# Kernel tuning notes

Measured on AMD Instinct MI355X. Metric: run time of the kernel, lower is better.

The kernel has to match this reference:

```python
import jax, jax.numpy as jnp
import numpy as np


def _local_similar(q, k, kH, kW):
    # q, k: [B, C, H, W] -> scores [B, H, W, kH*kW]
    # Matches similar_forward: zero-padded kH x kW neighborhood dot products.
    B, C, H, W = q.shape
    pH, pW = kH // 2, kW // 2
    kp = jnp.pad(k, ((0, 0), (0, 0), (pH, pH), (pW, pW)))
    scores = [
        jnp.einsum('bchw,bchw->bhw', q, kp[:, :, dh:dh + H, dw:dw + W])
        for dh in range(kH) for dw in range(kW)
    ]
    return jnp.stack(scores, axis=-1)


def _local_weighting(v, w, kH, kW):
    # v: [B, C, H, W], w: [B, H, W, kH*kW] -> out [B, C, H, W]
    # Matches weighting_forward: weighted sum over zero-padded neighborhood.
    B, C, H, W = v.shape
    pH, pW = kH // 2, kW // 2
    vp = jnp.pad(v, ((0, 0), (0, 0), (pH, pH), (pW, pW)))
    out = jnp.zeros_like(v)
    idx = 0
    for dh in range(kH):
        for dw in range(kW):
            out = out + w[..., idx][:, None, :, :] * vp[:, :, dh:dh + H, dw:dw + W]
            idx += 1
    return out


def setup_inputs() -> dict:
    key = jax.random.key(0)
    k1, k2, k3, k4 = jax.random.split(key, 4)
    B, C, H, W = 8, 64, 128, 128
    O = 64  # out_channels
    scale = 1.0 / np.sqrt(C).astype(np.float32)
    x = jax.random.normal(k1, (B, C, H, W), jnp.float32)
    W1 = jax.random.normal(k2, (O, C), jnp.float32) * scale  # conv1 (1x1, no bias)
    W2 = jax.random.normal(k3, (O, C), jnp.float32) * scale  # conv2
    W3 = jax.random.normal(k4, (O, C), jnp.float32) * scale  # conv3
    return {"x": x, "W1": W1, "W2": W2, "W3": W3, "kH": 7, "kW": 7}


def reference(x, W1, W2, W3, kH, kW):
    # 1x1 convs == per-pixel channel matmuls
    q = jnp.einsum('oc,bchw->bohw', W1, x)
    k = jnp.einsum('oc,bchw->bohw', W2, x)
    v = jnp.einsum('oc,bchw->bohw', W3, x)
    scores = _local_similar(q, k, kH, kW)          # [B, H, W, kH*kW]
    w = jax.nn.softmax(scores, axis=-1)
    return _local_weighting(v, w, kH, kW)          # [B, O, H, W]
```

## Files before the change

kernel.cpp:

```cpp
#include <hip/hip_runtime.h>
#include <hip/hip_bf16.h>

#define B_ 8
#define C_ 64
#define H_ 128
#define W_ 128
#define HW_ (H_ * W_)

typedef __attribute__((ext_vector_type(8))) short short8;
typedef __attribute__((ext_vector_type(4))) float float4v;
typedef _Float16 f16x2 __attribute__((ext_vector_type(2)));

static __device__ inline unsigned bfbits(float f) {
    __hip_bfloat16 h = __float2bfloat16(f);
    unsigned short s;
    __builtin_memcpy(&s, &h, 2);
    return (unsigned)s;
}

static __device__ inline float dot2(unsigned a, unsigned b, float c) {
    f16x2 ha, hb;
    __builtin_memcpy(&ha, &a, 4);
    __builtin_memcpy(&hb, &b, 4);
#if __has_builtin(__builtin_amdgcn_fdot2)
    return __builtin_amdgcn_fdot2(ha, hb, c, false);
#else
    return fmaf((float)ha.x, (float)hb.x, fmaf((float)ha.y, (float)hb.y, c));
#endif
}

static __device__ inline float2 up2(unsigned u) {
    f16x2 h;
    __builtin_memcpy(&h, &u, 4);
    return make_float2((float)h.x, (float)h.y);
}

__global__ void repack_w(const float* __restrict__ w1, const float* __restrict__ w2,
                         const float* __restrict__ w3,
                         unsigned short* __restrict__ wBhi, unsigned short* __restrict__ wBlo)
{
    const int i = blockIdx.x * 256 + threadIdx.x;
    if (i >= 12288) return;
    const int j = i & 7, lane = (i >> 3) & 63, ks = (i >> 9) & 1, nt = i >> 10;
    const int o = nt * 16 + (lane & 15);
    const int c = ks * 32 + (lane >> 4) * 8 + j;
    const float* wsel = (o < 64) ? w1 : (o < 128) ? w2 : w3;
    const float w = wsel[(o & 63) * 64 + c];
    const unsigned hb = bfbits(w);
    wBhi[i] = (unsigned short)hb;
    wBlo[i] = (unsigned short)bfbits(w - __uint_as_float(hb << 16));
}

__global__ __launch_bounds__(512, 4) void proj_qkv(
    const float* __restrict__ x,
    const unsigned short* __restrict__ wBhi, const unsigned short* __restrict__ wBlo,
    _Float16* __restrict__ q, _Float16* __restrict__ k, _Float16* __restrict__ v)
{
    const int b = blockIdx.y;
    const int px0 = blockIdx.x * 128;
    const int t = threadIdx.x;
    const int lane = t & 63;
    const int wave = t >> 6;
    const int wave_m = wave & 1, wave_n = wave >> 1;
    const int n = lane & 15, kg = lane >> 4;

    float4v acc[3][4];
    #pragma unroll
    for (int tnt = 0; tnt < 3; ++tnt)
        #pragma unroll
        for (int mt = 0; mt < 4; ++mt)
            acc[tnt][mt] = (float4v){0.f, 0.f, 0.f, 0.f};

    const float* xb = x + (size_t)b * C_ * HW_;
    const int pxl = px0 + wave_m * 64 + n;

    #pragma unroll
    for (int ks = 0; ks < 2; ++ks) {
        short8 ahi[4], alo[4];
        #pragma unroll
        for (int mt = 0; mt < 4; ++mt) {
            #pragma unroll
            for (int j = 0; j < 8; ++j) {
                const int c = ks * 32 + kg * 8 + j;
                const float f = xb[(size_t)c * HW_ + pxl + mt * 16];
                const unsigned hb = bfbits(f);
                ahi[mt][j] = (short)hb;
                alo[mt][j] = (short)bfbits(f - __uint_as_float(hb << 16));
            }
        }
        #pragma unroll
        for (int tnt = 0; tnt < 3; ++tnt) {
            const int gnt = wave_n * 3 + tnt;
            const size_t bidx = (((size_t)gnt * 2 + ks) * 64 + lane) * 8;
            short8 bh, bl;
            {
                const uint4 uh = *(const uint4*)(wBhi + bidx);
                const uint4 ul = *(const uint4*)(wBlo + bidx);
                __builtin_memcpy(&bh, &uh, 16);
                __builtin_memcpy(&bl, &ul, 16);
            }
            #pragma unroll
            for (int mt = 0; mt < 4; ++mt) {
                acc[tnt][mt] = __builtin_amdgcn_mfma_f32_16x16x32_bf16(
                    ahi[mt], bh, acc[tnt][mt], 0, 0, 0);
                acc[tnt][mt] = __builtin_amdgcn_mfma_f32_16x16x32_bf16(
                    alo[mt], bh, acc[tnt][mt], 0, 0, 0);
                acc[tnt][mt] = __builtin_amdgcn_mfma_f32_16x16x32_bf16(
                    ahi[mt], bl, acc[tnt][mt], 0, 0, 0);
            }
        }
    }

    #pragma unroll
    for (int tnt = 0; tnt < 3; ++tnt) {
        const int gnt = wave_n * 3 + tnt;
        _Float16* base = (gnt < 4) ? q : (gnt < 8) ? k : v;
        const int chunk = gnt & 3;
        #pragma unroll
        for (int mt = 0; mt < 4; ++mt) {
            const int pxm = px0 + wave_m * 64 + mt * 16 + kg * 4;
            const float4v d = acc[tnt][mt];
            _Float16* p = base + (((size_t)b * 4 + chunk) * HW_ + pxm) * 16 + n;
            #pragma unroll
            for (int r = 0; r < 4; ++r) p[(size_t)r * 16] = (_Float16)d[r];
        }
    }
}

#define HP_ 484
#define PL_ 1948

__global__ __launch_bounds__(512, 4) void local_attn(
    const _Float16* __restrict__ q, const _Float16* __restrict__ k,
    const _Float16* __restrict__ v, float* __restrict__ out)
{
    __shared__ float tile[8 * PL_];
    const int b = blockIdx.z, h0 = blockIdx.y * 16, w0 = blockIdx.x * 16;
    const int t = threadIdx.x;
    const int lane = t & 63, wave = t >> 6;
    const int g = lane & 1;
    const int pixel = wave * 32 + (lane >> 1);
    const int pw = pixel & 15, ph = pixel >> 4;
    const size_t px = (size_t)(h0 + ph) * W_ + (w0 + pw);

    uint4 qv[4];
    #pragma unroll
    for (int pp = 0; pp < 4; ++pp) {
        const int p8 = g * 4 + pp;
        qv[pp] = *(const uint4*)(q + (((size_t)b * 4 + (p8 >> 1)) * HW_ + px) * 16 + (p8 & 1) * 8);
    }

    for (int i = t; i < HP_ * 8; i += 512) {
        const int pix = i >> 3, c8 = i & 7;
        const int r = pix / 22, cl = pix - r * 22;
        const int gh = h0 + r - 3, gw = w0 + cl - 3;
        uint4 val = make_uint4(0u, 0u, 0u, 0u);
        if (gh >= 0 && gh < H_ && gw >= 0 && gw < W_)
            val = *(const uint4*)(k + (((size_t)b * 4 + (c8 >> 1)) * HW_ +
                                       (size_t)gh * W_ + gw) * 16 + (c8 & 1) * 8);
        *(uint4*)(tile + c8 * PL_ + pix * 4) = val;
    }
    __syncthreads();

    float sc[49];
    #pragma unroll
    for (int dh = 0; dh < 7; ++dh) {
        #pragma unroll
        for (int dw = 0; dw < 7; ++dw) {
            const int np = ((ph + dh) * 22 + (pw + dw)) * 4;
            float s0 = 0.f, s1 = 0.f, s2 = 0.f, s3 = 0.f;
            #pragma unroll
            for (int pp = 0; pp < 4; ++pp) {
                const uint4 u = *(const uint4*)(tile + (g * 4 + pp) * PL_ + np);
                s0 = dot2(qv[pp].x, u.x, s0);
                s1 = dot2(qv[pp].y, u.y, s1);
                s2 = dot2(qv[pp].z, u.z, s2);
                s3 = dot2(qv[pp].w, u.w, s3);
            }
            sc[dh * 7 + dw] = (s0 + s1) + (s2 + s3);
        }
    }

    #pragma unroll
    for (int i = 0; i < 49; ++i)
        sc[i] += __shfl_xor(sc[i], 1, 64);

    float m = sc[0];
    #pragma unroll
    for (int i = 1; i < 49; ++i) m = fmaxf(m, sc[i]);
    float s = 0.f;
    #pragma unroll
    for (int i = 0; i < 49; ++i) { sc[i] = __expf(sc[i] - m); s += sc[i]; }
    const float inv = 1.f / s;
    #pragma unroll
    for (int i = 0; i < 49; ++i) sc[i] *= inv;

    __syncthreads();

    for (int i = t; i < HP_ * 8; i += 512) {
        const int pix = i >> 3, c8 = i & 7;
        const int r = pix / 22, cl = pix - r * 22;
        const int gh = h0 + r - 3, gw = w0 + cl - 3;
        uint4 val = make_uint4(0u, 0u, 0u, 0u);
        if (gh >= 0 && gh < H_ && gw >= 0 && gw < W_)
            val = *(const uint4*)(v + (((size_t)b * 4 + (c8 >> 1)) * HW_ +
                                       (size_t)gh * W_ + gw) * 16 + (c8 & 1) * 8);
        *(uint4*)(tile + c8 * PL_ + pix * 4) = val;
    }
    __syncthreads();

    float acc[32];
    #pragma unroll
    for (int c = 0; c < 32; ++c) acc[c] = 0.f;
    #pragma unroll
    for (int dh = 0; dh < 7; ++dh) {
        #pragma unroll
        for (int dw = 0; dw < 7; ++dw) {
            const float wgt = sc[dh * 7 + dw];
            const int np = ((ph + dh) * 22 + (pw + dw)) * 4;
            #pragma unroll
            for (int pp = 0; pp < 4; ++pp) {
                const uint4 u = *(const uint4*)(tile + (g * 4 + pp) * PL_ + np);
                const int a = pp * 8;
                float2 f;
                f = up2(u.x); acc[a + 0] = fmaf(wgt, f.x, acc[a + 0]);
                              acc[a + 1] = fmaf(wgt, f.y, acc[a + 1]);
                f = up2(u.y); acc[a + 2] = fmaf(wgt, f.x, acc[a + 2]);
                              acc[a + 3] = fmaf(wgt, f.y, acc[a + 3]);
                f = up2(u.z); acc[a + 4] = fmaf(wgt, f.x, acc[a + 4]);
                              acc[a + 5] = fmaf(wgt, f.y, acc[a + 5]);
                f = up2(u.w); acc[a + 6] = fmaf(wgt, f.x, acc[a + 6]);
                              acc[a + 7] = fmaf(wgt, f.y, acc[a + 7]);
            }
        }
    }

    #pragma unroll
    for (int pp = 0; pp < 4; ++pp) {
        const int p8 = g * 4 + pp;
        const int ch0 = (p8 >> 1) * 16 + (p8 & 1) * 8;
        #pragma unroll
        for (int j = 0; j < 8; ++j)
            out[((size_t)b * 64 + ch0 + j) * HW_ + px] = acc[pp * 8 + j];
    }
}

extern "C" void kernel_launch(void* const* d_in, const int* in_sizes, int n_in,
                              void* d_out, int out_size, void* d_ws, size_t ws_size,
                              hipStream_t stream) {
    const float* x  = (const float*)d_in[0];
    const float* w1 = (const float*)d_in[1];
    const float* w2 = (const float*)d_in[2];
    const float* w3 = (const float*)d_in[3];

    const size_t NE = (size_t)B_ * 4 * HW_ * 16;
    _Float16* q = (_Float16*)d_ws;
    _Float16* k = q + NE;
    _Float16* v = k + NE;
    unsigned short* wBhi = (unsigned short*)(v + NE);
    unsigned short* wBlo = wBhi + 12288;
    float* o = (float*)d_out;

    repack_w<<<dim3(48), 256, 0, stream>>>(w1, w2, w3, wBhi, wBlo);
    proj_qkv<<<dim3(HW_ / 128, B_), 512, 0, stream>>>(x, wBhi, wBlo, q, k, v);
    local_attn<<<dim3(W_ / 16, H_ / 16, B_), 512, 0, stream>>>(q, k, v, o);
}
```

Before: 146.5 us.

## Stage x through LDS in projection and prefetch V tile during score compute

The projection kernel now loads the x tile with coalesced float4 reads into a padded LDS transpose buffer, replacing strided per-channel scalar global loads. In the attention kernel, the first 2048 elements of the V halo tile are loaded into registers before the score/softmax phase and written to LDS afterwards, overlapping global latency with compute. Costs are about 34KB extra LDS in the projection kernel, which may reduce occupancy, and 16 extra registers in the attention kernel alongside the 49 score and 32 accumulator registers.

```diff
diff --git a/kernel.cpp b/kernel.cpp
--- a/kernel.cpp
+++ b/kernel.cpp
@@ -51,11 +51,14 @@
     wBlo[i] = (unsigned short)bfbits(w - __uint_as_float(hb << 16));
 }
 
+#define XROW_ 68
+
 __global__ __launch_bounds__(512, 4) void proj_qkv(
     const float* __restrict__ x,
     const unsigned short* __restrict__ wBhi, const unsigned short* __restrict__ wBlo,
     _Float16* __restrict__ q, _Float16* __restrict__ k, _Float16* __restrict__ v)
 {
+    __shared__ float xt[128 * XROW_];
     const int b = blockIdx.y;
     const int px0 = blockIdx.x * 128;
     const int t = threadIdx.x;
@@ -64,6 +67,20 @@
     const int wave_m = wave & 1, wave_n = wave >> 1;
     const int n = lane & 15, kg = lane >> 4;
 
+    const float* xb = x + (size_t)b * C_ * HW_;
+    #pragma unroll
+    for (int r = 0; r < 4; ++r) {
+        const int fi = t + r * 512;
+        const int c = fi >> 5;
+        const int p4 = (fi & 31) * 4;
+        const float4 val = *(const float4*)(xb + (size_t)c * HW_ + px0 + p4);
+        xt[(p4 + 0) * XROW_ + c] = val.x;
+        xt[(p4 + 1) * XROW_ + c] = val.y;
+        xt[(p4 + 2) * XROW_ + c] = val.z;
+        xt[(p4 + 3) * XROW_ + c] = val.w;
+    }
+    __syncthreads();
+
     float4v acc[3][4];
     #pragma unroll
     for (int tnt = 0; tnt < 3; ++tnt)
@@ -71,18 +88,20 @@
         for (int mt = 0; mt < 4; ++mt)
             acc[tnt][mt] = (float4v){0.f, 0.f, 0.f, 0.f};
 
-    const float* xb = x + (size_t)b * C_ * HW_;
-    const int pxl = px0 + wave_m * 64 + n;
+    const int pxl = wave_m * 64 + n;
 
     #pragma unroll
     for (int ks = 0; ks < 2; ++ks) {
         short8 ahi[4], alo[4];
         #pragma unroll
         for (int mt = 0; mt < 4; ++mt) {
+            const float* xp = xt + (size_t)(pxl + mt * 16) * XROW_ + ks * 32 + kg * 8;
+            const float4 xa = *(const float4*)xp;
+            const float4 xc = *(const float4*)(xp + 4);
+            const float xv[8] = {xa.x, xa.y, xa.z, xa.w, xc.x, xc.y, xc.z, xc.w};
             #pragma unroll
             for (int j = 0; j < 8; ++j) {
-                const int c = ks * 32 + kg * 8 + j;
-                const float f = xb[(size_t)c * HW_ + pxl + mt * 16];
+                const float f = xv[j];
                 const unsigned hb = bfbits(f);
                 ahi[mt][j] = (short)hb;
                 alo[mt][j] = (short)bfbits(f - __uint_as_float(hb << 16));
@@ -162,6 +181,19 @@
     }
     __syncthreads();
 
+    uint4 vreg[4];
+    #pragma unroll
+    for (int r = 0; r < 4; ++r) {
+        const int i = t + r * 512;
+        const int pix = i >> 3, c8 = i & 7;
+        const int rr = pix / 22, cl = pix - rr * 22;
+        const int gh = h0 + rr - 3, gw = w0 + cl - 3;
+        vreg[r] = make_uint4(0u, 0u, 0u, 0u);
+        if (gh >= 0 && gh < H_ && gw >= 0 && gw < W_)
+            vreg[r] = *(const uint4*)(v + (((size_t)b * 4 + (c8 >> 1)) * HW_ +
+                                           (size_t)gh * W_ + gw) * 16 + (c8 & 1) * 8);
+    }
+
     float sc[49];
     #pragma unroll
     for (int dh = 0; dh < 7; ++dh) {
@@ -197,7 +229,13 @@
 
     __syncthreads();
 
-    for (int i = t; i < HP_ * 8; i += 512) {
+    #pragma unroll
+    for (int r = 0; r < 4; ++r) {
+        const int i = t + r * 512;
+        const int pix = i >> 3, c8 = i & 7;
+        *(uint4*)(tile + c8 * PL_ + pix * 4) = vreg[r];
+    }
+    for (int i = t + 2048; i < HP_ * 8; i += 512) {
         const int pix = i >> 3, c8 = i & 7;
         const int r = pix / 22, cl = pix - r * 22;
         const int gh = h0 + r - 3, gw = w0 + cl - 3;
```

Result: faster. 142.6 us (-2.7%).
